# Performance work log

Measured on AMD Instinct MI355X. Metric: run time of the kernel, lower is better.

The kernel has to match this reference:

```python
import jax, jax.numpy as jnp
import numpy as np

B, S, D, H = 2, 2048, 2048, 16
HD = D // H  # 128
L = 10  # adapter_len


def setup_inputs() -> dict:
    key = jax.random.key(0)
    ks = jax.random.split(key, 8)
    x = jax.random.normal(ks[0], (B, S, D), dtype=jnp.float32)
    wq = jax.random.normal(ks[1], (D, D), dtype=jnp.float32) * 0.02
    wk = jax.random.normal(ks[2], (D, D), dtype=jnp.float32) * 0.02
    wv = jax.random.normal(ks[3], (D, D), dtype=jnp.float32) * 0.02
    wo = jax.random.normal(ks[4], (D, D), dtype=jnp.float32) * 0.02
    adapter = jax.random.normal(ks[5], (1, L, D), dtype=jnp.float32)
    gate = jax.random.normal(ks[6], (1, H, 1, 1), dtype=jnp.float32) * 0.1
    # rotary frequencies (LLaMA style, theta=10000)
    inv_freq = 1.0 / (10000.0 ** (jnp.arange(0, HD, 2, dtype=jnp.float32) / HD))
    t = jnp.arange(S, dtype=jnp.float32)
    ang = jnp.outer(t, inv_freq)  # [S, HD//2]
    freqs_cos = jnp.cos(ang)
    freqs_sin = jnp.sin(ang)
    # additive causal mask [1,1,S,S]
    mask = jnp.triu(jnp.full((S, S), -1e9, dtype=jnp.float32), k=1)[None, None]
    return {"x": x, "wq": wq, "wk": wk, "wv": wv, "wo": wo,
            "adapter": adapter, "gate": gate,
            "freqs_cos": freqs_cos, "freqs_sin": freqs_sin, "mask": mask}


def _rope(v, cos, sin):
    # v: [B,S,H,HD]; cos/sin: [S, HD//2]; complex multiply on (even, odd) pairs
    v = v.reshape(*v.shape[:-1], HD // 2, 2)
    v0, v1 = v[..., 0], v[..., 1]
    c = cos[None, :, None, :]
    s = sin[None, :, None, :]
    out = jnp.stack([v0 * c - v1 * s, v0 * s + v1 * c], axis=-1)
    return out.reshape(*out.shape[:-2], HD)


def reference(x, wq, wk, wv, wo, adapter, gate, freqs_cos, freqs_sin, mask):
    scale = 1.0 / np.sqrt(HD)
    xq = (x @ wq).reshape(B, S, H, HD)
    xk = (x @ wk).reshape(B, S, H, HD)
    xv = (x @ wv).reshape(B, S, H, HD)
    xq = _rope(xq, freqs_cos, freqs_sin)
    xk = _rope(xk, freqs_cos, freqs_sin)
    # self-attention with additive causal mask
    scores = jnp.einsum('bqhd,bkhd->bhqk', xq, xk) * scale + mask
    probs = jax.nn.softmax(scores.astype(jnp.float32), axis=-1).astype(xq.dtype)
    out = jnp.einsum('bhqk,bkhd->bqhd', probs, xv)  # [B,S,H,HD]
    # gated adapter cross-attention (no rotary on adapter K/V)
    ak = (adapter[0] @ wk).reshape(L, H, HD)
    av = (adapter[0] @ wv).reshape(L, H, HD)
    a_scores = jnp.einsum('bqhd,khd->bhqk', xq, ak) * scale
    a_probs = gate * jax.nn.softmax(a_scores.astype(jnp.float32), axis=-1).astype(xq.dtype)
    out = out + jnp.einsum('bhqk,khd->bqhd', a_probs, av)
    return out.reshape(B, S, D) @ wo
```

## Files before the change

kernel.cpp:

```cpp
#include <hip/hip_runtime.h>


typedef unsigned short ushort_t;
typedef unsigned int uint32;
typedef __attribute__((ext_vector_type(8))) short bf16x8;
typedef __attribute__((ext_vector_type(4))) float f32x4;

__device__ __forceinline__ void async16(void* lds, const void* g) {
  __builtin_amdgcn_global_load_lds((const __attribute__((address_space(1))) void*)g,
                                   (__attribute__((address_space(3))) void*)lds,
                                   16, 0, 0);
}
__device__ __forceinline__ ushort_t f2bf(float f) {
  uint32 u = __float_as_uint(f);
  u += 0x7FFFu + ((u >> 16) & 1u);
  return (ushort_t)(u >> 16);
}
__device__ __forceinline__ float bf2f(ushort_t b) {
  return __uint_as_float(((uint32)b) << 16);
}
__device__ __forceinline__ float dpp_xor1(float v) {
  return __int_as_float(__builtin_amdgcn_update_dpp(
      0, __float_as_int(v), 0xB1, 0xf, 0xf, true));
}
#define DPP_MAX(t, ctrl) \
  t = fmaxf(t, __int_as_float(__builtin_amdgcn_update_dpp( \
      0, __float_as_int(t), (ctrl), 0xf, 0xf, true)))
#define DPP_ADD(t, ctrl) \
  t += __int_as_float(__builtin_amdgcn_update_dpp( \
      0, __float_as_int(t), (ctrl), 0xf, 0xf, true))
__device__ __forceinline__ float rowmax16(float t) {
  DPP_MAX(t, 0xB1);
  DPP_MAX(t, 0x4E);
  t = fmaxf(t, __int_as_float(__builtin_amdgcn_ds_swizzle(
      __float_as_int(t), 0x101F)));
  DPP_MAX(t, 0x128);
  return t;
}
__device__ __forceinline__ float rowsum16(float t) {
  DPP_ADD(t, 0xB1);
  DPP_ADD(t, 0x4E);
  t += __int_as_float(__builtin_amdgcn_ds_swizzle(__float_as_int(t), 0x101F));
  DPP_ADD(t, 0x128);
  return t;
}

__global__ __launch_bounds__(256) void cast_x_kernel(const float* __restrict__ x,
                                                     ushort_t* __restrict__ Xb) {
  size_t i = ((size_t)blockIdx.x * 256 + threadIdx.x) * 8;
  float4 a = *(const float4*)(x + i);
  float4 b = *(const float4*)(x + i + 4);
  uint4 o;
  o.x = (uint32)f2bf(a.x) | ((uint32)f2bf(a.y) << 16);
  o.y = (uint32)f2bf(a.z) | ((uint32)f2bf(a.w) << 16);
  o.z = (uint32)f2bf(b.x) | ((uint32)f2bf(b.y) << 16);
  o.w = (uint32)f2bf(b.z) | ((uint32)f2bf(b.w) << 16);
  *(uint4*)(Xb + i) = o;
}

__global__ __launch_bounds__(256) void rope_pack_kernel(
    const float* __restrict__ fc, const float* __restrict__ fs,
    float2* __restrict__ fcs) {
  int i = blockIdx.x * 256 + threadIdx.x;
  fcs[i] = make_float2(fc[i], fs[i]);
}

__global__ __launch_bounds__(256) void transpose_w_kernel(
    const float* __restrict__ w0, const float* __restrict__ w1,
    const float* __restrict__ w2, const float* __restrict__ w3,
    ushort_t* __restrict__ outBase) {
  const float* W = (blockIdx.z == 0) ? w0 : (blockIdx.z == 1) ? w1
                 : (blockIdx.z == 2) ? w2 : w3;
  ushort_t* Wt = outBase + (size_t)blockIdx.z * 4194304;
  __shared__ float L[64][65];
  int t = threadIdx.x, tc = t & 63, tr = t >> 6;
  int k0 = blockIdx.x * 64, n0 = blockIdx.y * 64;
  for (int i = 0; i < 16; ++i) {
    int r = i * 4 + tr;
    L[r][tc] = W[(size_t)(k0 + r) * 2048 + n0 + tc];
  }
  __syncthreads();
  int tr8 = t >> 5, tc2 = t & 31;
  for (int i = 0; i < 8; ++i) {
    int r = i * 8 + tr8;
    uint32 pk = (uint32)f2bf(L[2 * tc2][r]) | ((uint32)f2bf(L[2 * tc2 + 1][r]) << 16);
    *(uint32*)(Wt + (size_t)(n0 + r) * 2048 + k0 + 2 * tc2) = pk;
  }
}

__global__ __launch_bounds__(256) void adapter_kv_kernel(
    const float* __restrict__ adapter, const float* __restrict__ wk,
    const float* __restrict__ wv, float* __restrict__ ak, float* __restrict__ av) {
  const float* W = blockIdx.z ? wv : wk;
  float* out = blockIdx.z ? av : ak;
  __shared__ float As[10][128];
  int t = threadIdx.x;
  int k0 = blockIdx.y * 128;
  for (int i = t; i < 1280; i += 256)
    As[i >> 7][i & 127] = adapter[(size_t)(i >> 7) * 2048 + k0 + (i & 127)];
  __syncthreads();
  int n = blockIdx.x * 256 + t;
  float acc[10];
#pragma unroll
  for (int l = 0; l < 10; ++l) acc[l] = 0.f;
  for (int kk = 0; kk < 128; ++kk) {
    float wv_ = W[(size_t)(k0 + kk) * 2048 + n];
#pragma unroll
    for (int l = 0; l < 10; ++l) acc[l] += As[l][kk] * wv_;
  }
#pragma unroll
  for (int l = 0; l < 10; ++l) atomicAdd(&out[l * 2048 + n], acc[l]);
}

__global__ __launch_bounds__(256) void adapter_pack_kernel(
    const float* __restrict__ ak, const float* __restrict__ av,
    ushort_t* __restrict__ akb, ushort_t* __restrict__ avb) {
  int t = blockIdx.x * 256 + threadIdx.x;
  if (t < 32768) {
    int h = t >> 11, l = (t >> 7) & 15, d = t & 127;
    akb[t] = (l < 10) ? f2bf(ak[l * 2048 + h * 128 + d]) : (ushort_t)0;
  }
  int h = t >> 12, d = (t >> 5) & 127, l = t & 31;
  avb[t] = (l < 10) ? f2bf(av[l * 2048 + h * 128 + d]) : (ushort_t)0;
}

#define QK_BARX() asm volatile("s_barrier" ::: "memory")
#define QK_LGKM0() asm volatile("s_waitcnt lgkmcnt(0)" ::: "memory")

__device__ __forceinline__ void kloop_128x256(
    char* lds, const ushort_t* __restrict__ A, const ushort_t* __restrict__ Bt,
    size_t bm0, size_t bn0, f32x4 (&acc)[4][4]) {
  const int tid = (int)threadIdx.x;
  const int w = tid >> 6, lane = tid & 63, quad = lane >> 4, l15 = lane & 15;
  const int wr = (w >> 2) * 64, wc = (w & 3) * 64;
  const int nt = 32;
  char* const pA0 = lds;
  char* const pA1 = lds + 16384;
  char* const pB0 = lds + 32768;
  char* const pB1 = lds + 65536;

#define PAT(T) (((T) & 1) ? pA1 : pA0)
#define PBT(T) (((T) & 1) ? pB1 : pB0)
#define SEGL(OP, LDSB, GROW, T)                                                \
  do {                                                                         \
    int rr_ = w * 8 + (lane >> 3);                                             \
    int cl_ = (lane & 7) ^ (rr_ & 7);                                          \
    async16((LDSB) + w * 1024,                                                 \
            (OP) + ((GROW) + (size_t)rr_) * 2048 + (size_t)((T) * 64 + cl_ * 8)); \
  } while (0)
#define ST_A(T)                                                                \
  do { if ((T) < nt) { SEGL(A, PAT(T), bm0, (T));                              \
                       SEGL(A, PAT(T) + 8192, bm0 + 64, (T)); } } while (0)
#define ST_B0(T)                                                               \
  do { if ((T) < nt) SEGL(Bt, PBT(T), bn0, (T)); } while (0)
#define ST_B123(T)                                                             \
  do { if ((T) < nt) { SEGL(Bt, PBT(T) + 8192,  bn0 + 64,  (T));               \
                       SEGL(Bt, PBT(T) + 16384, bn0 + 128, (T));               \
                       SEGL(Bt, PBT(T) + 24576, bn0 + 192, (T)); } } while (0)

  ST_A(0); ST_B0(0); ST_B123(0); ST_B123(1);
  asm volatile("s_waitcnt vmcnt(3)" ::: "memory");
  QK_BARX();

#pragma unroll 2
  for (int t = 0; t < nt; ++t) {
    const char* pA = PAT(t);
    const char* pB = PBT(t);
    bf16x8 bfv[4][2];
#pragma unroll
    for (int j = 0; j < 4; ++j) {
      int brow = wc + j * 16 + l15;
#pragma unroll
      for (int ks = 0; ks < 2; ++ks)
        bfv[j][ks] = *(const bf16x8*)(pB + brow * 128 +
                                      (((ks * 4 + quad) ^ (brow & 7)) * 16));
    }
#pragma unroll
    for (int ph = 0; ph < 2; ++ph) {
      bf16x8 af[2][2];
#pragma unroll
      for (int ii = 0; ii < 2; ++ii) {
        int arow = wr + (ph * 2 + ii) * 16 + l15;
#pragma unroll
        for (int ks = 0; ks < 2; ++ks)
          af[ii][ks] = *(const bf16x8*)(pA + arow * 128 +
                                        (((ks * 4 + quad) ^ (arow & 7)) * 16));
      }
      if (ph == 0) { ST_A(t + 1); ST_B0(t + 1); }
      else         { ST_B123(t + 2); }
      QK_BARX();
      QK_LGKM0();
      __builtin_amdgcn_s_setprio(1);
#pragma unroll
      for (int ks = 0; ks < 2; ++ks)
#pragma unroll
        for (int ii = 0; ii < 2; ++ii)
#pragma unroll
          for (int j = 0; j < 4; ++j)
            acc[ph * 2 + ii][j] = __builtin_amdgcn_mfma_f32_16x16x32_bf16(
                af[ii][ks], bfv[j][ks], acc[ph * 2 + ii][j], 0, 0, 0);
      __builtin_amdgcn_s_setprio(0);
      if (ph == 1) {
        if (t == nt - 2) asm volatile("s_waitcnt vmcnt(0)" ::: "memory");
        else             asm volatile("s_waitcnt vmcnt(3)" ::: "memory");
      }
      QK_BARX();
    }
  }
#undef PAT
#undef PBT
#undef SEGL
#undef ST_A
#undef ST_B0
#undef ST_B123
}

__global__ __launch_bounds__(512, 2) void gemm_qkv128_kernel(
    const ushort_t* __restrict__ A, const ushort_t* __restrict__ Bt,
    ushort_t* __restrict__ outQ, ushort_t* __restrict__ outK,
    ushort_t* __restrict__ Vt, const float2* __restrict__ fcs) {
  __shared__ char lds[98304];
  const int tid = (int)threadIdx.x;
  const int w = tid >> 6, lane = tid & 63, quad = lane >> 4, l15 = lane & 15;
  const int wr = (w >> 2) * 64, wc = (w & 3) * 64;

  const int wg = ((int)blockIdx.x & 7) * 96 + ((int)blockIdx.x >> 3);
  const size_t bm0 = (size_t)(wg & 31) * 128;
  const size_t bn0 = (size_t)(wg >> 5) * 256;

  f32x4 acc[4][4];
  f32x4 z4 = {0.f, 0.f, 0.f, 0.f};
#pragma unroll
  for (int i = 0; i < 4; ++i)
#pragma unroll
    for (int j = 0; j < 4; ++j) acc[i][j] = z4;

  kloop_128x256(lds, A, Bt, bm0, bn0, acc);

  const int seg = (int)(bn0 >> 11);
  if (seg < 2) {
    ushort_t* ob = seg ? outK : outQ;
#pragma unroll
    for (int i = 0; i < 4; ++i)
#pragma unroll
      for (int r = 0; r < 4; ++r) {
        size_t m = bm0 + wr + i * 16 + quad * 4 + r;
        int s = (int)(m & 2047);
#pragma unroll
        for (int j = 0; j < 4; ++j) {
          size_t n = (bn0 + wc + j * 16 + l15) & 2047;
          float v = acc[i][j][r];
          float v2 = dpp_xor1(v);
          int fi = ((int)n & 127) >> 1;
          float2 cs = fcs[s * 64 + fi];
          v = (lane & 1) ? (v2 * cs.y + v * cs.x) : (v * cs.x - v2 * cs.y);
          ob[m * 2048 + n] = f2bf(v);
        }
      }
  } else {
    char* T = lds + w * 8192;
#pragma unroll
    for (int i = 0; i < 4; ++i)
#pragma unroll
      for (int j = 0; j < 4; ++j) {
        int nn = j * 16 + l15;
        int md0 = i * 8 + quad * 2;
        uint32 p01 = (uint32)f2bf(acc[i][j][0]) | ((uint32)f2bf(acc[i][j][1]) << 16);
        uint32 p23 = (uint32)f2bf(acc[i][j][2]) | ((uint32)f2bf(acc[i][j][3]) << 16);
        *(uint32*)(T + nn * 128 + ((md0 ^ (nn & 31)) * 4)) = p01;
        *(uint32*)(T + nn * 128 + (((md0 + 1) ^ (nn & 31)) * 4)) = p23;
      }
    const int b = (int)(bm0 >> 11);
    const int s0 = (int)(bm0 & 2047) + wr;
    const int n2 = (int)(bn0 & 2047) + wc;
#pragma unroll
    for (int it = 0; it < 32; ++it) {
      int row = it * 2 + (lane >> 5);
      int pp = lane & 31;
      uint32 dv = *(const uint32*)(T + row * 128 + pp * 4);
      int md = pp ^ (row & 31);
      int nloc = n2 + row;
      size_t bh = (size_t)b * 16 + (nloc >> 7);
      *(uint32*)(Vt + (bh * 128 + (size_t)(nloc & 127)) * 2048 + s0 + 2 * md) = dv;
    }
  }
}

__global__ __launch_bounds__(512, 2) void gemm_wo_kernel(
    const ushort_t* __restrict__ A, const ushort_t* __restrict__ Bt,
    float* __restrict__ out) {
  __shared__ char lds[98304];
  const int tid = (int)threadIdx.x;
  const int w = tid >> 6, lane = tid & 63, quad = lane >> 4, l15 = lane & 15;
  const int wr = (w >> 2) * 64, wc = (w & 3) * 64;

  const int wg = ((int)blockIdx.x & 7) * 32 + ((int)blockIdx.x >> 3);
  const size_t bm0 = (size_t)(wg & 31) * 128;
  const size_t bn0 = (size_t)(wg >> 5) * 256;

  f32x4 acc[4][4];
  f32x4 z4 = {0.f, 0.f, 0.f, 0.f};
#pragma unroll
  for (int i = 0; i < 4; ++i)
#pragma unroll
    for (int j = 0; j < 4; ++j) acc[i][j] = z4;

  kloop_128x256(lds, A, Bt, bm0, bn0, acc);

#pragma unroll
  for (int i = 0; i < 4; ++i)
#pragma unroll
    for (int r = 0; r < 4; ++r) {
      size_t m = bm0 + wr + i * 16 + quad * 4 + r;
#pragma unroll
      for (int j = 0; j < 4; ++j) {
        size_t n = bn0 + wc + j * 16 + l15;
        out[m * 2048 + n] = acc[i][j][r];
      }
    }
}

__global__ __launch_bounds__(256, 4) void flash_kernel(
    const ushort_t* __restrict__ Qb, const ushort_t* __restrict__ Kb,
    const ushort_t* __restrict__ Vt, const ushort_t* __restrict__ akb,
    const ushort_t* __restrict__ avb, const float* __restrict__ gate,
    ushort_t* __restrict__ Ob) {
  __shared__ char ldsK[16384];
  __shared__ char ldsV[16384];
  __shared__ char ldsP[8192];
  const int tid = threadIdx.x;
  const int w = tid >> 6, lane = tid & 63, quad = lane >> 4, l15 = lane & 15;
  const int idx = blockIdx.x;
  const int pg = idx >> 8, c = idx & 255;
  const int u = c >> 3, vv = c & 7;
  const int uu = (pg & 2) ? ((u + 16) & 31) : u;
  const int qt2 = (pg & 1) ? (31 - uu) : uu;
  const int hb = (pg << 3) | vv;
  const int h = hb >> 1, b = hb & 1;
  const float scale = 0.08838834764831845f;

  bf16x8 ones;
#pragma unroll
  for (int j = 0; j < 8; ++j) ones[j] = (short)0x3F80;

  bf16x8 qf[4];
  {
    size_t qrow = (size_t)qt2 * 64 + w * 16 + l15;
    const ushort_t* base = Qb + ((size_t)b * 2048 + qrow) * 2048 + h * 128 + quad * 8;
#pragma unroll
    for (int ds = 0; ds < 4; ++ds) qf[ds] = *(const bf16x8*)(base + ds * 32);
  }

  f32x4 zero4 = {0.f, 0.f, 0.f, 0.f};
  f32x4 oacc[8];
  f32x4 osum = zero4;
  float mrow[4];
#pragma unroll
  for (int n8 = 0; n8 < 8; ++n8) oacc[n8] = zero4;
#pragma unroll
  for (int r = 0; r < 4; ++r) mrow[r] = -1e30f;

  for (int kt = 0; kt <= qt2; ++kt) {
#pragma unroll
    for (int ii = 0; ii < 4; ++ii) {
      int r0 = w * 16 + ii * 4;
      int row = r0 + (lane >> 4);
      int cl = (lane & 15) ^ (row & 15);
      async16(ldsK + r0 * 256,
              Kb + ((size_t)b * 2048 + kt * 64 + row) * 2048 + h * 128 + cl * 8);
    }
#pragma unroll
    for (int ii = 0; ii < 4; ++ii) {
      int d0 = w * 32 + ii * 8;
      int dr = d0 + (lane >> 3);
      int cl = (lane & 7) ^ (dr & 7);
      async16(ldsV + d0 * 128,
              Vt + ((size_t)(b * 16 + h) * 128 + dr) * 2048 + kt * 64 + cl * 8);
    }
    __syncthreads();

    f32x4 sacc[4];
#pragma unroll
    for (int nt = 0; nt < 4; ++nt) sacc[nt] = zero4;
#pragma unroll
    for (int ds = 0; ds < 4; ++ds) {
      bf16x8 kf[4];
      int ch = ds * 4 + quad;
#pragma unroll
      for (int nt = 0; nt < 4; ++nt) {
        int row = nt * 16 + l15;
        kf[nt] = *(const bf16x8*)(ldsK + row * 256 + ((ch ^ (row & 15)) * 16));
      }
#pragma unroll
      for (int nt = 0; nt < 4; ++nt)
        sacc[nt] = __builtin_amdgcn_mfma_f32_16x16x32_bf16(qf[ds], kf[nt], sacc[nt], 0, 0, 0);
    }

    const bool domask = (kt == qt2);
    float tmax[4] = {-1e30f, -1e30f, -1e30f, -1e30f};
    const int qbr = qt2 * 64 + w * 16 + quad * 4;
#pragma unroll
    for (int nt = 0; nt < 4; ++nt) {
      int kg = kt * 64 + nt * 16 + l15;
#pragma unroll
      for (int r = 0; r < 4; ++r) {
        float s = sacc[nt][r] * scale;
        if (domask && kg > qbr + r) s = -1e30f;
        sacc[nt][r] = s;
        tmax[r] = fmaxf(tmax[r], s);
      }
    }
    float need = 0.f;
#pragma unroll
    for (int r = 0; r < 4; ++r) {
      tmax[r] = rowmax16(tmax[r]);
      need = fmaxf(need, tmax[r] - mrow[r]);
    }
    if (__any(need > 8.0f)) {
      float alpha[4];
#pragma unroll
      for (int r = 0; r < 4; ++r) {
        float mnew = fmaxf(mrow[r], tmax[r]);
        alpha[r] = __expf(mrow[r] - mnew);
        osum[r] *= alpha[r];
        mrow[r] = mnew;
      }
#pragma unroll
      for (int n8 = 0; n8 < 8; ++n8)
#pragma unroll
        for (int r = 0; r < 4; ++r) oacc[n8][r] *= alpha[r];
    }
    uint32 pk[4][4];
#pragma unroll
    for (int nt = 0; nt < 4; ++nt)
#pragma unroll
      for (int r = 0; r < 4; ++r) {
        float pv = __expf(sacc[nt][r] - mrow[r]);
        float pn = dpp_xor1(pv);
        uint32 d_;
        asm volatile("v_cvt_pk_bf16_f32 %0, %1, %2" : "=v"(d_) : "v"(pv), "v"(pn));
        pk[nt][r] = d_;
      }
    if (!(lane & 1)) {
#pragma unroll
      for (int nt = 0; nt < 4; ++nt)
#pragma unroll
        for (int r = 0; r < 4; ++r) {
          int col = nt * 16 + l15;
          int prow = w * 16 + quad * 4 + r;
          *(uint32*)(ldsP + prow * 128 + (((col >> 3) ^ (prow & 7)) * 16) + (col & 7) * 2) = pk[nt][r];
        }
    }

#pragma unroll
    for (int ks = 0; ks < 2; ++ks) {
      int ch = ks * 4 + quad;
      int prow = w * 16 + l15;
      bf16x8 pf = *(const bf16x8*)(ldsP + prow * 128 + ((ch ^ (prow & 7)) * 16));
      osum = __builtin_amdgcn_mfma_f32_16x16x32_bf16(pf, ones, osum, 0, 0, 0);
#pragma unroll
      for (int n8 = 0; n8 < 8; ++n8) {
        int dr = n8 * 16 + l15;
        bf16x8 vf = *(const bf16x8*)(ldsV + dr * 128 + ((ch ^ (dr & 7)) * 16));
        oacc[n8] = __builtin_amdgcn_mfma_f32_16x16x32_bf16(pf, vf, oacc[n8], 0, 0, 0);
      }
    }
    __syncthreads();
  }

  const float g = gate[h];
  {
    int row = w * 16 + (lane >> 2);
    *(uint2*)(ldsP + row * 80 + 32 + (lane & 3) * 8) = make_uint2(0, 0);
  }
  f32x4 sa = zero4;
#pragma unroll
  for (int ds = 0; ds < 4; ++ds) {
    bf16x8 kfa = *(const bf16x8*)(akb + ((size_t)h * 16 + l15) * 128 + ds * 32 + quad * 8);
    sa = __builtin_amdgcn_mfma_f32_16x16x32_bf16(qf[ds], kfa, sa, 0, 0, 0);
  }
#pragma unroll
  for (int r = 0; r < 4; ++r) {
    float s = sa[r] * scale;
    if (l15 >= 10) s = -1e30f;
    float mx = rowmax16(s);
    float e = __expf(s - mx);
    float sum = rowsum16(e);
    float pv = g * e / sum;
    int row = w * 16 + quad * 4 + r;
    *(ushort_t*)(ldsP + row * 80 + l15 * 2) = f2bf(pv);
  }
  bf16x8 paf = *(const bf16x8*)(ldsP + (w * 16 + l15) * 80 + quad * 16);

  float rl[4];
#pragma unroll
  for (int r = 0; r < 4; ++r) rl[r] = 1.f / osum[r];
#pragma unroll
  for (int n8 = 0; n8 < 8; ++n8)
#pragma unroll
    for (int r = 0; r < 4; ++r) oacc[n8][r] *= rl[r];
#pragma unroll
  for (int n8 = 0; n8 < 8; ++n8) {
    bf16x8 avf = *(const bf16x8*)(avb + ((size_t)h * 128 + n8 * 16 + l15) * 32 + quad * 8);
    oacc[n8] = __builtin_amdgcn_mfma_f32_16x16x32_bf16(paf, avf, oacc[n8], 0, 0, 0);
  }
  size_t qb0 = (size_t)qt2 * 64 + w * 16 + quad * 4;
#pragma unroll
  for (int n8 = 0; n8 < 8; ++n8) {
    size_t col = (size_t)h * 128 + n8 * 16 + l15;
#pragma unroll
    for (int r = 0; r < 4; ++r)
      Ob[((size_t)b * 2048 + qb0 + r) * 2048 + col] = f2bf(oacc[n8][r]);
  }
}

extern "C" void kernel_launch(void* const* d_in, const int* in_sizes, int n_in,
                              void* d_out, int out_size, void* d_ws, size_t ws_size,
                              hipStream_t stream) {
  (void)in_sizes; (void)n_in; (void)out_size; (void)ws_size;
  const float* x       = (const float*)d_in[0];
  const float* wq      = (const float*)d_in[1];
  const float* wk      = (const float*)d_in[2];
  const float* wv      = (const float*)d_in[3];
  const float* wo      = (const float*)d_in[4];
  const float* adapter = (const float*)d_in[5];
  const float* gate    = (const float*)d_in[6];
  const float* fc      = (const float*)d_in[7];
  const float* fs      = (const float*)d_in[8];

  char* ws = (char*)d_ws;
  ushort_t* Xb   = (ushort_t*)(ws + 0);
  ushort_t* WtQ  = (ushort_t*)(ws + 16777216);
  ushort_t* WtO  = (ushort_t*)(ws + 41943040);
  ushort_t* Qb   = (ushort_t*)(ws + 50331648);
  ushort_t* Kb   = (ushort_t*)(ws + 67108864);
  ushort_t* Vt   = (ushort_t*)(ws + 83886080);
  float*    ak   = (float*)   (ws + 100663296);
  float*    av   = (float*)   (ws + 100745216);
  ushort_t* akb  = (ushort_t*)(ws + 100827136);
  ushort_t* avb  = (ushort_t*)(ws + 100892672);
  float2*   fcs  = (float2*)  (ws + 101023744);
  ushort_t* Ob   = Xb;

  cast_x_kernel<<<4096, 256, 0, stream>>>(x, Xb);
  rope_pack_kernel<<<512, 256, 0, stream>>>(fc, fs, fcs);
  transpose_w_kernel<<<dim3(32, 32, 4), 256, 0, stream>>>(wq, wk, wv, wo, WtQ);
  hipMemsetAsync(ak, 0, 163840, stream);
  adapter_kv_kernel<<<dim3(8, 16, 2), 256, 0, stream>>>(adapter, wk, wv, ak, av);
  adapter_pack_kernel<<<256, 256, 0, stream>>>(ak, av, akb, avb);
  gemm_qkv128_kernel<<<dim3(768), 512, 0, stream>>>(Xb, WtQ, Qb, Kb, Vt, fcs);
  flash_kernel<<<dim3(1024), 256, 0, stream>>>(Qb, Kb, Vt, akb, avb, gate, Ob);
  gemm_wo_kernel<<<dim3(256), 512, 0, stream>>>(Ob, WtO, (float*)d_out);
}
```

Baseline: 432.6 us.

## Load GEMM A fragments directly from global, drop rope pack and adapter atomics

The shared GEMM k-loop no longer stages the A operand through LDS. Each wave loads its A fragments straight from global memory into registers, double-buffered across tiles, which cuts LDS to 64 KB per block. The rope_pack kernel is removed and the QKV epilogue reads cos and sin directly. The adapter K/V projection now loops over K inside each block instead of using a memset plus atomics. The aim is fewer launches and less LDS traffic, at the cost of uncoalesced global reads for A and much less parallelism in the adapter kernel (16 blocks).

```diff
diff --git a/kernel.cpp b/kernel.cpp
--- a/kernel.cpp
+++ b/kernel.cpp
@@ -58,13 +58,6 @@
   *(uint4*)(Xb + i) = o;
 }
 
-__global__ __launch_bounds__(256) void rope_pack_kernel(
-    const float* __restrict__ fc, const float* __restrict__ fs,
-    float2* __restrict__ fcs) {
-  int i = blockIdx.x * 256 + threadIdx.x;
-  fcs[i] = make_float2(fc[i], fs[i]);
-}
-
 __global__ __launch_bounds__(256) void transpose_w_kernel(
     const float* __restrict__ w0, const float* __restrict__ w1,
     const float* __restrict__ w2, const float* __restrict__ w3,
@@ -95,21 +88,23 @@
   float* out = blockIdx.z ? av : ak;
   __shared__ float As[10][128];
   int t = threadIdx.x;
-  int k0 = blockIdx.y * 128;
-  for (int i = t; i < 1280; i += 256)
-    As[i >> 7][i & 127] = adapter[(size_t)(i >> 7) * 2048 + k0 + (i & 127)];
-  __syncthreads();
   int n = blockIdx.x * 256 + t;
   float acc[10];
 #pragma unroll
   for (int l = 0; l < 10; ++l) acc[l] = 0.f;
-  for (int kk = 0; kk < 128; ++kk) {
-    float wv_ = W[(size_t)(k0 + kk) * 2048 + n];
-#pragma unroll
-    for (int l = 0; l < 10; ++l) acc[l] += As[l][kk] * wv_;
-  }
-#pragma unroll
-  for (int l = 0; l < 10; ++l) atomicAdd(&out[l * 2048 + n], acc[l]);
+  for (int k0 = 0; k0 < 2048; k0 += 128) {
+    __syncthreads();
+    for (int i = t; i < 1280; i += 256)
+      As[i >> 7][i & 127] = adapter[(size_t)(i >> 7) * 2048 + k0 + (i & 127)];
+    __syncthreads();
+    for (int kk = 0; kk < 128; ++kk) {
+      float wv_ = W[(size_t)(k0 + kk) * 2048 + n];
+#pragma unroll
+      for (int l = 0; l < 10; ++l) acc[l] += As[l][kk] * wv_;
+    }
+  }
+#pragma unroll
+  for (int l = 0; l < 10; ++l) out[l * 2048 + n] = acc[l];
 }
 
 __global__ __launch_bounds__(256) void adapter_pack_kernel(
@@ -125,7 +120,6 @@
 }
 
 #define QK_BARX() asm volatile("s_barrier" ::: "memory")
-#define QK_LGKM0() asm volatile("s_waitcnt lgkmcnt(0)" ::: "memory")
 
 __device__ __forceinline__ void kloop_128x256(
     char* lds, const ushort_t* __restrict__ A, const ushort_t* __restrict__ Bt,
@@ -134,92 +128,92 @@
   const int w = tid >> 6, lane = tid & 63, quad = lane >> 4, l15 = lane & 15;
   const int wr = (w >> 2) * 64, wc = (w & 3) * 64;
   const int nt = 32;
-  char* const pA0 = lds;
-  char* const pA1 = lds + 16384;
-  char* const pB0 = lds + 32768;
-  char* const pB1 = lds + 65536;
-
-#define PAT(T) (((T) & 1) ? pA1 : pA0)
+  char* const pB0 = lds;
+  char* const pB1 = lds + 32768;
+  const ushort_t* aBase = A + (bm0 + wr + l15) * 2048;
+
 #define PBT(T) (((T) & 1) ? pB1 : pB0)
-#define SEGL(OP, LDSB, GROW, T)                                                \
+#define SEGB(LDSB, GROW, T)                                                    \
   do {                                                                         \
     int rr_ = w * 8 + (lane >> 3);                                             \
     int cl_ = (lane & 7) ^ (rr_ & 7);                                          \
     async16((LDSB) + w * 1024,                                                 \
-            (OP) + ((GROW) + (size_t)rr_) * 2048 + (size_t)((T) * 64 + cl_ * 8)); \
+            Bt + ((GROW) + (size_t)rr_) * 2048 + (size_t)((T) * 64 + cl_ * 8)); \
   } while (0)
-#define ST_A(T)                                                                \
-  do { if ((T) < nt) { SEGL(A, PAT(T), bm0, (T));                              \
-                       SEGL(A, PAT(T) + 8192, bm0 + 64, (T)); } } while (0)
 #define ST_B0(T)                                                               \
-  do { if ((T) < nt) SEGL(Bt, PBT(T), bn0, (T)); } while (0)
+  do { if ((T) < nt) SEGB(PBT(T), bn0, (T)); } while (0)
 #define ST_B123(T)                                                             \
-  do { if ((T) < nt) { SEGL(Bt, PBT(T) + 8192,  bn0 + 64,  (T));               \
-                       SEGL(Bt, PBT(T) + 16384, bn0 + 128, (T));               \
-                       SEGL(Bt, PBT(T) + 24576, bn0 + 192, (T)); } } while (0)
-
-  ST_A(0); ST_B0(0); ST_B123(0); ST_B123(1);
+  do { if ((T) < nt) { SEGB(PBT(T) + 8192,  bn0 + 64,  (T));                   \
+                       SEGB(PBT(T) + 16384, bn0 + 128, (T));                   \
+                       SEGB(PBT(T) + 24576, bn0 + 192, (T)); } } while (0)
+#define LD_A(DST, T)                                                           \
+  do { if ((T) < nt) {                                                         \
+    _Pragma("unroll") for (int ii_ = 0; ii_ < 4; ++ii_)                        \
+      _Pragma("unroll") for (int ks_ = 0; ks_ < 2; ++ks_)                      \
+        DST[ii_][ks_] = *(const bf16x8*)(aBase + ii_ * 32768 +                 \
+                          (size_t)((T) * 64) + (ks_ * 4 + quad) * 8);          \
+  } } while (0)
+
+  bf16x8 afA[4][2], afB[4][2];
+
+  ST_B0(0); ST_B123(0);
+  LD_A(afA, 0);
+  ST_B123(1);
   asm volatile("s_waitcnt vmcnt(3)" ::: "memory");
   QK_BARX();
 
-#pragma unroll 2
-  for (int t = 0; t < nt; ++t) {
-    const char* pA = PAT(t);
-    const char* pB = PBT(t);
-    bf16x8 bfv[4][2];
-#pragma unroll
-    for (int j = 0; j < 4; ++j) {
-      int brow = wc + j * 16 + l15;
-#pragma unroll
-      for (int ks = 0; ks < 2; ++ks)
-        bfv[j][ks] = *(const bf16x8*)(pB + brow * 128 +
-                                      (((ks * 4 + quad) ^ (brow & 7)) * 16));
-    }
-#pragma unroll
-    for (int ph = 0; ph < 2; ++ph) {
-      bf16x8 af[2][2];
-#pragma unroll
-      for (int ii = 0; ii < 2; ++ii) {
-        int arow = wr + (ph * 2 + ii) * 16 + l15;
-#pragma unroll
-        for (int ks = 0; ks < 2; ++ks)
-          af[ii][ks] = *(const bf16x8*)(pA + arow * 128 +
-                                        (((ks * 4 + quad) ^ (arow & 7)) * 16));
-      }
-      if (ph == 0) { ST_A(t + 1); ST_B0(t + 1); }
-      else         { ST_B123(t + 2); }
-      QK_BARX();
-      QK_LGKM0();
-      __builtin_amdgcn_s_setprio(1);
-#pragma unroll
-      for (int ks = 0; ks < 2; ++ks)
-#pragma unroll
-        for (int ii = 0; ii < 2; ++ii)
-#pragma unroll
-          for (int j = 0; j < 4; ++j)
-            acc[ph * 2 + ii][j] = __builtin_amdgcn_mfma_f32_16x16x32_bf16(
-                af[ii][ks], bfv[j][ks], acc[ph * 2 + ii][j], 0, 0, 0);
-      __builtin_amdgcn_s_setprio(0);
-      if (ph == 1) {
-        if (t == nt - 2) asm volatile("s_waitcnt vmcnt(0)" ::: "memory");
-        else             asm volatile("s_waitcnt vmcnt(3)" ::: "memory");
-      }
-      QK_BARX();
-    }
-  }
-#undef PAT
-#undef PBT
-#undef SEGL
-#undef ST_A
+#define TILE(T, CUR, NXT)                                                      \
+  do {                                                                         \
+    const char* pB = PBT(T);                                                   \
+    bf16x8 bfv[4][2];                                                          \
+    _Pragma("unroll") for (int j_ = 0; j_ < 4; ++j_) {                         \
+      int brow_ = wc + j_ * 16 + l15;                                          \
+      _Pragma("unroll") for (int ks_ = 0; ks_ < 2; ++ks_)                      \
+        bfv[j_][ks_] = *(const bf16x8*)(pB + brow_ * 128 +                     \
+                         (((ks_ * 4 + quad) ^ (brow_ & 7)) * 16));             \
+    }                                                                          \
+    ST_B0((T) + 1);                                                            \
+    LD_A(NXT, (T) + 1);                                                        \
+    QK_BARX();                                                                 \
+    __builtin_amdgcn_s_setprio(1);                                             \
+    _Pragma("unroll") for (int ks_ = 0; ks_ < 2; ++ks_)                        \
+      _Pragma("unroll") for (int ii_ = 0; ii_ < 2; ++ii_)                      \
+        _Pragma("unroll") for (int j_ = 0; j_ < 4; ++j_)                       \
+          acc[ii_][j_] = __builtin_amdgcn_mfma_f32_16x16x32_bf16(              \
+              CUR[ii_][ks_], bfv[j_][ks_], acc[ii_][j_], 0, 0, 0);             \
+    __builtin_amdgcn_s_setprio(0);                                             \
+    QK_BARX();                                                                 \
+    ST_B123((T) + 2);                                                          \
+    __builtin_amdgcn_s_setprio(1);                                             \
+    _Pragma("unroll") for (int ks_ = 0; ks_ < 2; ++ks_)                        \
+      _Pragma("unroll") for (int ii_ = 2; ii_ < 4; ++ii_)                      \
+        _Pragma("unroll") for (int j_ = 0; j_ < 4; ++j_)                       \
+          acc[ii_][j_] = __builtin_amdgcn_mfma_f32_16x16x32_bf16(              \
+              CUR[ii_][ks_], bfv[j_][ks_], acc[ii_][j_], 0, 0, 0);             \
+    __builtin_amdgcn_s_setprio(0);                                             \
+    if ((T) == nt - 2) asm volatile("s_waitcnt vmcnt(0)" ::: "memory");        \
+    else               asm volatile("s_waitcnt vmcnt(3)" ::: "memory");        \
+    QK_BARX();                                                                 \
+  } while (0)
+
+  for (int t = 0; t < nt; t += 2) {
+    TILE(t, afA, afB);
+    TILE(t + 1, afB, afA);
+  }
+#undef TILE
+#undef LD_A
 #undef ST_B0
 #undef ST_B123
+#undef SEGB
+#undef PBT
 }
 
 __global__ __launch_bounds__(512, 2) void gemm_qkv128_kernel(
     const ushort_t* __restrict__ A, const ushort_t* __restrict__ Bt,
     ushort_t* __restrict__ outQ, ushort_t* __restrict__ outK,
-    ushort_t* __restrict__ Vt, const float2* __restrict__ fcs) {
-  __shared__ char lds[98304];
+    ushort_t* __restrict__ Vt,
+    const float* __restrict__ fc, const float* __restrict__ fs) {
+  __shared__ char lds[65536];
   const int tid = (int)threadIdx.x;
   const int w = tid >> 6, lane = tid & 63, quad = lane >> 4, l15 = lane & 15;
   const int wr = (w >> 2) * 64, wc = (w & 3) * 64;
@@ -252,8 +246,9 @@
           float v = acc[i][j][r];
           float v2 = dpp_xor1(v);
           int fi = ((int)n & 127) >> 1;
-          float2 cs = fcs[s * 64 + fi];
-          v = (lane & 1) ? (v2 * cs.y + v * cs.x) : (v * cs.x - v2 * cs.y);
+          float cosv = fc[s * 64 + fi];
+          float sinv = fs[s * 64 + fi];
+          v = (lane & 1) ? (v2 * sinv + v * cosv) : (v * cosv - v2 * sinv);
           ob[m * 2048 + n] = f2bf(v);
         }
       }
@@ -289,7 +284,7 @@
 __global__ __launch_bounds__(512, 2) void gemm_wo_kernel(
     const ushort_t* __restrict__ A, const ushort_t* __restrict__ Bt,
     float* __restrict__ out) {
-  __shared__ char lds[98304];
+  __shared__ char lds[65536];
   const int tid = (int)threadIdx.x;
   const int w = tid >> 6, lane = tid & 63, quad = lane >> 4, l15 = lane & 15;
   const int wr = (w >> 2) * 64, wc = (w & 3) * 64;
@@ -539,16 +534,13 @@
   float*    av   = (float*)   (ws + 100745216);
   ushort_t* akb  = (ushort_t*)(ws + 100827136);
   ushort_t* avb  = (ushort_t*)(ws + 100892672);
-  float2*   fcs  = (float2*)  (ws + 101023744);
   ushort_t* Ob   = Xb;
 
   cast_x_kernel<<<4096, 256, 0, stream>>>(x, Xb);
-  rope_pack_kernel<<<512, 256, 0, stream>>>(fc, fs, fcs);
   transpose_w_kernel<<<dim3(32, 32, 4), 256, 0, stream>>>(wq, wk, wv, wo, WtQ);
-  hipMemsetAsync(ak, 0, 163840, stream);
-  adapter_kv_kernel<<<dim3(8, 16, 2), 256, 0, stream>>>(adapter, wk, wv, ak, av);
+  adapter_kv_kernel<<<dim3(8, 1, 2), 256, 0, stream>>>(adapter, wk, wv, ak, av);
   adapter_pack_kernel<<<256, 256, 0, stream>>>(ak, av, akb, avb);
-  gemm_qkv128_kernel<<<dim3(768), 512, 0, stream>>>(Xb, WtQ, Qb, Kb, Vt, fcs);
+  gemm_qkv128_kernel<<<dim3(768), 512, 0, stream>>>(Xb, WtQ, Qb, Kb, Vt, fc, fs);
   flash_kernel<<<dim3(1024), 256, 0, stream>>>(Qb, Kb, Vt, akb, avb, gate, Ob);
   gemm_wo_kernel<<<dim3(256), 512, 0, stream>>>(Ob, WtO, (float*)d_out);
 }
```

New measurement: 814.8 us. 1.88x slower.
